# Kernel optimization log

Hardware: AMD Instinct MI355X
Metric: run time of the kernel (lower is better)

Reference implementation:

```python
import jax, jax.numpy as jnp
import numpy as np

B, L, D, H, DH, DFF, NL, A = 32, 1024, 512, 8, 64, 2048, 6, 21
CL = 4  # new variables per clique (chain junction tree)


def _build_mask():
    # Mirrors _make_junction_tree_mask: each position attends to itself,
    # to all parent-clique variables, and to earlier vars in its own clique.
    m = np.zeros((L, L), dtype=bool)
    for c in range(L // CL):
        own = range(c * CL, (c + 1) * CL)
        par = range((c - 1) * CL, c * CL) if c > 0 else range(0)
        for i in own:
            m[i, i] = True
            for p in par:
                m[i, p] = True
            for v in own:
                if v < i:
                    m[i, v] = True
    return m


def setup_inputs() -> dict:
    key = jax.random.key(0)
    ks = jax.random.split(key, 12)
    s = 0.02
    inp = {
        "x": jax.random.randint(ks[0], (B, L), 0, A, dtype=jnp.int32),
        "mask": jnp.asarray(_build_mask())[None, None],  # (1,1,L,L), broadcasts over B,H
        "tok_emb": jax.random.normal(ks[1], (A, D)) * s,
        "pos_emb": jax.random.normal(ks[2], (L, D)) * s,
        "wq": jax.random.normal(ks[3], (NL, D, D)) * s,
        "bq": jnp.zeros((NL, D)),
        "wk": jax.random.normal(ks[4], (NL, D, D)) * s,
        "bk": jnp.zeros((NL, D)),
        "wv": jax.random.normal(ks[5], (NL, D, D)) * s,
        "bv": jnp.zeros((NL, D)),
        "wo": jax.random.normal(ks[6], (NL, D, D)) * s,
        "bo": jnp.zeros((NL, D)),
        "ln1_s": jnp.ones((NL, D)),
        "ln1_b": jnp.zeros((NL, D)),
        "ln2_s": jnp.ones((NL, D)),
        "ln2_b": jnp.zeros((NL, D)),
        "w1": jax.random.normal(ks[7], (NL, D, DFF)) * s,
        "b1": jnp.zeros((NL, DFF)),
        "w2": jax.random.normal(ks[8], (NL, DFF, D)) * s,
        "b2": jnp.zeros((NL, D)),
        "wout": jax.random.normal(ks[9], (D, A)) * s,
        "bout": jnp.zeros((A,)),
    }
    return inp


def _ln(x, s, b):
    mu = x.mean(-1, keepdims=True)
    var = ((x - mu) ** 2).mean(-1, keepdims=True)
    return (x - mu) * jax.lax.rsqrt(var + 1e-6) * s + b


def reference(x, mask, tok_emb, pos_emb, wq, bq, wk, bk, wv, bv, wo, bo,
              ln1_s, ln1_b, ln2_s, ln2_b, w1, b1, w2, b2, wout, bout):
    h = tok_emb[x] + pos_emb[None, :, :]           # (B, L, D)
    neg = jnp.asarray(-1e9, h.dtype)
    scale = jnp.asarray(1.0 / np.sqrt(DH), h.dtype)
    for l in range(NL):
        # masked multi-head self-attention (pre-LN block)
        hn = _ln(h, ln1_s[l], ln1_b[l])
        q = (hn @ wq[l] + bq[l]).reshape(B, L, H, DH)
        k = (hn @ wk[l] + bk[l]).reshape(B, L, H, DH)
        v = (hn @ wv[l] + bv[l]).reshape(B, L, H, DH)
        sc = jnp.einsum('blhd,bmhd->bhlm', q, k) * scale
        sc = jnp.where(mask, sc, neg)              # junction-tree sparsity pattern
        attn = jax.nn.softmax(sc, axis=-1)
        o = jnp.einsum('bhlm,bmhd->blhd', attn, v).reshape(B, L, D) @ wo[l] + bo[l]
        h = h + o
        # feed-forward
        hn = _ln(h, ln2_s[l], ln2_b[l])
        h = h + (jax.nn.gelu(hn @ w1[l] + b1[l]) @ w2[l] + b2[l])
    return h @ wout + bout                          # (B, L, alphabet_size)
```

## Files before the change

### kernel.cpp

```cpp
#include <hip/hip_runtime.h>

#define BB 32
#define LL 1024
#define DD 512
#define HH 8
#define DHH 64
#define DFF 2048
#define NLAYERS 6
#define AA 21
#define MTOT (BB*LL)
#define QS 1536

typedef unsigned short u16;
typedef __bf16 bf16x8 __attribute__((ext_vector_type(8)));
typedef float f32x4 __attribute__((ext_vector_type(4)));
typedef u16 u16x8 __attribute__((ext_vector_type(8)));

__device__ __forceinline__ float bf2f(u16 u) {
    return __uint_as_float(((unsigned int)u) << 16);
}
__device__ __forceinline__ u16 f2bf(float f) {
    unsigned int i = __float_as_uint(f);
    unsigned int r = i + 0x7FFFu + ((i >> 16) & 1u);
    return (u16)(r >> 16);
}

__global__ void detect_kernel(const void* __restrict__ tok, int* __restrict__ flag) {
    __shared__ int cnt[256];
    int t = threadIdx.x;
    const u16* p = (const u16*)tok;
    int c = 0;
    #pragma unroll
    for (int j = 0; j < 8; j++) {
        u16 u = p[2 * (t * 8 + j)];
        int e = (u >> 7) & 0xFF;
        c += (e >= 97 && e <= 137) ? 1 : 0;
    }
    cnt[t] = c;
    __syncthreads();
    for (int s = 128; s; s >>= 1) {
        if (t < s) cnt[t] += cnt[t + s];
        __syncthreads();
    }
    if (t == 0) flag[0] = (cnt[0] > 1024) ? 1 : 0;
}

#define NTAB 13
struct ConvTab {
    const void* src[NTAB];
    unsigned long long dstOff[NTAB];
    int n[NTAB];
    int chunk[NTAB];
    int lstride[NTAB];
};
__global__ __launch_bounds__(256) void conv_small(ConvTab tab, u16* __restrict__ spBase,
                                                  const int* __restrict__ flag, int total) {
    int i = blockIdx.x * 256 + threadIdx.x;
    if (i >= total) return;
    int fl = flag[0];
    #pragma unroll 1
    for (int e = 0; e < NTAB; e++) {
        if (i < tab.n[e]) {
            const void* s = tab.src[e];
            u16 val = fl ? ((const u16*)s)[i] : f2bf(((const float*)s)[i]);
            int c = i / tab.chunk[e];
            int r = i - c * tab.chunk[e];
            spBase[tab.dstOff[e] + (size_t)c * tab.lstride[e] + r] = val;
            return;
        }
        i -= tab.n[e];
    }
}

__global__ __launch_bounds__(256) void conv_T(const void* __restrict__ src,
                                              u16* __restrict__ dst, int R, int C,
                                              const int* __restrict__ flag, int dstZS) {
    __shared__ u16 tile[32][33];
    int z = blockIdx.z;
    size_t zoffS = (size_t)z * R * C;
    size_t zoffD = (size_t)z * dstZS;
    int bx = blockIdx.x * 32, by = blockIdx.y * 32;
    int tx = threadIdx.x & 31, ty = threadIdx.x >> 5;
    int fl = flag[0];
    const u16* s16 = (const u16*)src + zoffS;
    const float* s32 = (const float*)src + zoffS;
    #pragma unroll
    for (int r = 0; r < 4; r++) {
        size_t idx = (size_t)(by + ty * 4 + r) * C + bx + tx;
        tile[ty * 4 + r][tx] = fl ? s16[idx] : f2bf(s32[idx]);
    }
    __syncthreads();
    #pragma unroll
    for (int r = 0; r < 4; r++)
        dst[zoffD + (size_t)(bx + ty * 4 + r) * R + by + tx] = tile[tx][ty * 4 + r];
}

__global__ __launch_bounds__(256) void woutpad_kernel(const void* __restrict__ wout,
                                                      const void* __restrict__ bout,
                                                      u16* __restrict__ wpad,
                                                      u16* __restrict__ bpad,
                                                      const int* __restrict__ flag) {
    int i = blockIdx.x * 256 + threadIdx.x;
    int fl = flag[0];
    if (i < 128 * 512) {
        int n = i >> 9, kk = i & 511;
        u16 val = 0;
        if (n < AA) val = fl ? ((const u16*)wout)[kk * AA + n] : f2bf(((const float*)wout)[kk * AA + n]);
        wpad[(size_t)n * 512 + kk] = val;
    }
    if (i < 128) {
        u16 val = 0;
        if (i < AA) val = fl ? ((const u16*)bout)[i] : f2bf(((const float*)bout)[i]);
        bpad[i] = val;
    }
}

__global__ __launch_bounds__(128) void embed_kernel(const int* __restrict__ x,
                                                    const u16* __restrict__ tok_emb,
                                                    const u16* __restrict__ pos_emb,
                                                    float* __restrict__ h) {
    int row = blockIdx.x;
    int l = row & (LL - 1);
    int tok = x[row];
    int c = threadIdx.x * 4;
    ushort4 te = *(const ushort4*)(tok_emb + (size_t)tok * DD + c);
    ushort4 pe = *(const ushort4*)(pos_emb + (size_t)l * DD + c);
    float4 o;
    o.x = bf2f(te.x) + bf2f(pe.x);
    o.y = bf2f(te.y) + bf2f(pe.y);
    o.z = bf2f(te.z) + bf2f(pe.z);
    o.w = bf2f(te.w) + bf2f(pe.w);
    *(float4*)(h + (size_t)row * DD + c) = o;
}

__global__ __launch_bounds__(256) void ln_kernel(const float* __restrict__ h,
                                                 const u16* __restrict__ s,
                                                 const u16* __restrict__ b,
                                                 u16* __restrict__ outp) {
    int row = blockIdx.x * 4 + (threadIdx.x >> 6);
    int lane = threadIdx.x & 63;
    const float* hr = h + (size_t)row * DD + lane * 8;
    f32x4 v0 = *(const f32x4*)hr;
    f32x4 v1 = *(const f32x4*)(hr + 4);
    float sum = v0[0]+v0[1]+v0[2]+v0[3]+v1[0]+v1[1]+v1[2]+v1[3];
    #pragma unroll
    for (int off = 32; off; off >>= 1) sum += __shfl_xor(sum, off, 64);
    float mu = sum * (1.0f / DD);
    float var = 0.f;
    #pragma unroll
    for (int i = 0; i < 4; i++) {
        float d0 = v0[i] - mu, d1 = v1[i] - mu;
        var += d0 * d0 + d1 * d1;
    }
    #pragma unroll
    for (int off = 32; off; off >>= 1) var += __shfl_xor(var, off, 64);
    float rs = rsqrtf(var * (1.0f / DD) + 1e-6f);
    u16x8 sv = *(const u16x8*)(s + lane * 8);
    u16x8 bv = *(const u16x8*)(b + lane * 8);
    u16x8 o;
    #pragma unroll
    for (int i = 0; i < 8; i++) {
        float xv = (i < 4) ? v0[i] : v1[i - 4];
        o[i] = f2bf((xv - mu) * rs * bf2f(sv[i]) + bf2f(bv[i]));
    }
    *(u16x8*)(outp + (size_t)row * DD + lane * 8) = o;
}

#define GLD16(gp, lp) __builtin_amdgcn_global_load_lds( \
    (const __attribute__((address_space(1))) void*)(gp), \
    (__attribute__((address_space(3))) void*)(lp), 16, 0, 0)

template <int EPI>
__global__ __launch_bounds__(256) void gemm_bt(const u16* __restrict__ A,
                                               const u16* __restrict__ BT,
                                               const u16* __restrict__ bias,
                                               u16* __restrict__ Cb,
                                               float* __restrict__ Cf,
                                               int M, int N, int K, int lda,
                                               const int* __restrict__ flag) {
    __shared__ __align__(16) u16 Als[2][128 * 32];
    __shared__ __align__(16) u16 Bls[2][128 * 32];
    const int tid  = threadIdx.x;
    const int lane = tid & 63;
    const int wave = tid >> 6;

    int gx = gridDim.x, gy = gridDim.y;
    int tileX, tileY;
    if ((gy & 7) == 0) {
        int bid = blockIdx.y * gx + blockIdx.x;
        int xcd = bid & 7;
        int idx = bid >> 3;
        int stripe = gy >> 3;
        tileX = idx % gx;
        tileY = xcd * stripe + idx / gx;
    } else {
        tileX = blockIdx.x; tileY = blockIdx.y;
    }
    const int tileM = tileY * 128;
    const int tileN = tileX * 128;
    const int wm = (wave & 1) * 64;
    const int wn = (wave >> 1) * 64;

    const int srow = tid >> 2;
    const int scol = (((tid & 3) ^ ((tid >> 3) & 3))) * 8;

    const u16* Ag0 = A  + (size_t)(tileM + srow) * lda + scol;
    const u16* Ag1 = A  + (size_t)(tileM + 64 + srow) * lda + scol;
    const u16* Bg0 = BT + (size_t)(tileN + srow) * K + scol;
    const u16* Bg1 = BT + (size_t)(tileN + 64 + srow) * K + scol;

    f32x4 acc[4][4] = {};
    const int lm = lane & 15;
    const int lk = (((lane >> 4) ^ ((lm >> 1) & 3))) * 8;

    const int nk = K >> 5;
    GLD16(Ag0, Als[0] + tid * 8);
    GLD16(Ag1, Als[0] + 2048 + tid * 8);
    GLD16(Bg0, Bls[0] + tid * 8);
    GLD16(Bg1, Bls[0] + 2048 + tid * 8);
    __syncthreads();

    for (int kt = 0; kt < nk; kt++) {
        const int cur = kt & 1;
        const int nxt = cur ^ 1;
        if (kt + 1 < nk) {
            const int k1 = (kt + 1) << 5;
            GLD16(Ag0 + k1, Als[nxt] + tid * 8);
            GLD16(Ag1 + k1, Als[nxt] + 2048 + tid * 8);
            GLD16(Bg0 + k1, Bls[nxt] + tid * 8);
            GLD16(Bg1 + k1, Bls[nxt] + 2048 + tid * 8);
        }
        bf16x8 af[4], bfr[4];
        #pragma unroll
        for (int i = 0; i < 4; i++)
            af[i] = *(const bf16x8*)(Als[cur] + (wm + i * 16 + lm) * 32 + lk);
        #pragma unroll
        for (int j = 0; j < 4; j++)
            bfr[j] = *(const bf16x8*)(Bls[cur] + (wn + j * 16 + lm) * 32 + lk);
        #pragma unroll
        for (int i = 0; i < 4; i++)
            #pragma unroll
            for (int j = 0; j < 4; j++)
                acc[i][j] = __builtin_amdgcn_mfma_f32_16x16x32_bf16(af[i], bfr[j], acc[i][j], 0, 0, 0);
        __syncthreads();
    }

    int fl = 0;
    if constexpr (EPI == 3) fl = flag[0];
    const int r0 = (lane >> 4) * 4;
    #pragma unroll
    for (int j = 0; j < 4; j++) {
        int col = tileN + wn + j * 16 + lm;
        float bv = bf2f(bias[col]);
        #pragma unroll
        for (int i = 0; i < 4; i++) {
            int row = tileM + wm + i * 16 + r0;
            #pragma unroll
            for (int r = 0; r < 4; r++) {
                float xv = acc[i][j][r] + bv;
                if constexpr (EPI == 0) {
                    Cb[(size_t)(row + r) * N + col] = f2bf(xv);
                } else if constexpr (EPI == 1) {
                    float u = 1.5957691216057308f * (xv + 0.044715f * xv * xv * xv);
                    float t = 1.0f - 2.0f / (__expf(u) + 1.0f);
                    Cb[(size_t)(row + r) * N + col] = f2bf(0.5f * xv * (1.0f + t));
                } else if constexpr (EPI == 2) {
                    Cf[(size_t)(row + r) * N + col] += xv;
                } else if constexpr (EPI == 4) {
                    size_t idx = (size_t)(row + r) * N + col;
                    Cb[idx] = f2bf(xv + Cf[idx]);
                } else {
                    if (col < AA) {
                        size_t idx = (size_t)(row + r) * AA + col;
                        if (fl) Cb[idx] = f2bf(xv);
                        else    Cf[idx] = xv;
                    }
                }
            }
        }
    }
}

__global__ __launch_bounds__(256) void attn_kernel(u16* qkv) {
    int bl   = blockIdx.x * 4 + (threadIdx.x >> 6);
    int lane = threadIdx.x & 63;
    int l    = bl & (LL - 1);
    int lo   = (l & ~3) - 4; if (lo < 0) lo = 0;
    int nj   = l - lo + 1;

    size_t qrow = (size_t)bl * QS;
    int off = lane * 8;

    u16x8 q8 = *(const u16x8*)(qkv + qrow + off);
    float qf[8];
    #pragma unroll
    for (int i = 0; i < 8; i++) qf[i] = bf2f(q8[i]) * 0.125f;

    size_t base = (size_t)(bl - (l - lo)) * QS;
    float sc[8];
    u16x8 v8[8];
    #pragma unroll
    for (int j = 0; j < 8; j++) {
        int jc = (j < nj) ? j : (nj - 1);
        const u16* krow = qkv + base + (size_t)jc * QS;
        u16x8 k8 = *(const u16x8*)(krow + 512 + off);
        v8[j]    = *(const u16x8*)(krow + 1024 + off);
        float t = 0.f;
        #pragma unroll
        for (int i = 0; i < 8; i++) t = fmaf(qf[i], bf2f(k8[i]), t);
        t += __shfl_xor(t, 1, 64);
        t += __shfl_xor(t, 2, 64);
        t += __shfl_xor(t, 4, 64);
        sc[j] = (j < nj) ? t : -1e30f;
    }
    float m = sc[0];
    #pragma unroll
    for (int j = 1; j < 8; j++) m = fmaxf(m, sc[j]);
    float p[8], den = 0.f;
    #pragma unroll
    for (int j = 0; j < 8; j++) { p[j] = __expf(sc[j] - m); den += p[j]; }
    float inv = 1.0f / den;
    float o[8] = {};
    #pragma unroll
    for (int j = 0; j < 8; j++)
        #pragma unroll
        for (int i = 0; i < 8; i++) o[i] = fmaf(p[j], bf2f(v8[j][i]), o[i]);
    u16x8 ov;
    #pragma unroll
    for (int i = 0; i < 8; i++) ov[i] = f2bf(o[i] * inv);
    *(u16x8*)(qkv + qrow + off) = ov;
}

extern "C" void kernel_launch(void* const* d_in, const int* in_sizes, int n_in,
                              void* d_out, int out_size, void* d_ws, size_t ws_size,
                              hipStream_t stream) {
    const int base = n_in - 22;
    const int*  x    = (const int*)d_in[0];
    const void* tokI = d_in[2 + base];
    const void* posI = d_in[3 + base];
    const void* wqI  = d_in[4 + base];
    const void* bqI  = d_in[5 + base];
    const void* wkI  = d_in[6 + base];
    const void* bkI  = d_in[7 + base];
    const void* wvI  = d_in[8 + base];
    const void* bvI  = d_in[9 + base];
    const void* woI  = d_in[10 + base];
    const void* boI  = d_in[11 + base];
    const void* ln1sI = d_in[12 + base];
    const void* ln1bI = d_in[13 + base];
    const void* ln2sI = d_in[14 + base];
    const void* ln2bI = d_in[15 + base];
    const void* w1I  = d_in[16 + base];
    const void* b1I  = d_in[17 + base];
    const void* w2I  = d_in[18 + base];
    const void* b2I  = d_in[19 + base];
    const void* woutI = d_in[20 + base];
    const void* boutI = d_in[21 + base];

    char* ws = (char*)d_ws;
    float* h   = (float*)(ws + 0);
    u16*  hn   = (u16*)(ws + 67108864);
    u16*  qkv  = (u16*)(ws + 100663296);
    u16*  wT   = (u16*)(ws + 201326592);
    u16*  sp   = (u16*)(ws + 239075328);
    int* flag  = (int*)(ws + 240500736);

    u16* mid = qkv;

    u16* wqkvT = wT;
    u16* woT   = wT + 4718592;
    u16* w1T   = wT + 6291456;
    u16* w2T   = wT + 12582912;

    const unsigned long long oWoutPad = 0;
    const unsigned long long oBoutPad = 65536;
    const unsigned long long oTok     = 65664;
    const unsigned long long oPos     = 76416;
    const unsigned long long oQkvB    = 600704;
    const unsigned long long oBo      = 609920;
    const unsigned long long oB1      = 612992;
    const unsigned long long oB2      = 625280;
    const unsigned long long oLn1s    = 628352;
    const unsigned long long oLn1b    = 631424;
    const unsigned long long oLn2s    = 634496;
    const unsigned long long oLn2b    = 637568;

    detect_kernel<<<1, 256, 0, stream>>>(tokI, flag);

    ConvTab tab;
    const void* srcs[NTAB] = {tokI, bqI, bkI, bvI, boI, b1I, b2I, ln1sI, ln1bI, ln2sI, ln2bI, posI, tokI};
    unsigned long long offs[NTAB] = {oTok, oQkvB, oQkvB + 512, oQkvB + 1024, oBo, oB1, oB2,
                                     oLn1s, oLn1b, oLn2s, oLn2b, oPos, oTok};
    int ns[NTAB]     = {10752, 3072, 3072, 3072, 3072, 12288, 3072, 3072, 3072, 3072, 3072, 524288, 0};
    int chunks[NTAB] = {10752, 512, 512, 512, 3072, 12288, 3072, 3072, 3072, 3072, 3072, 524288, 1};
    int lstr[NTAB]   = {10752, 1536, 1536, 1536, 3072, 12288, 3072, 3072, 3072, 3072, 3072, 524288, 1};
    int total = 0;
    for (int e = 0; e < NTAB; e++) {
        tab.src[e] = srcs[e]; tab.dstOff[e] = offs[e]; tab.n[e] = ns[e];
        tab.chunk[e] = chunks[e]; tab.lstride[e] = lstr[e];
        total += ns[e];
    }
    conv_small<<<(total + 255) / 256, 256, 0, stream>>>(tab, sp, flag, total);
    woutpad_kernel<<<256, 256, 0, stream>>>(woutI, boutI, sp + oWoutPad, sp + oBoutPad, flag);

    conv_T<<<dim3(16, 16, 6), 256, 0, stream>>>(wqI, wqkvT,          DD, DD, flag, 786432);
    conv_T<<<dim3(16, 16, 6), 256, 0, stream>>>(wkI, wqkvT + 262144, DD, DD, flag, 786432);
    conv_T<<<dim3(16, 16, 6), 256, 0, stream>>>(wvI, wqkvT + 524288, DD, DD, flag, 786432);
    conv_T<<<dim3(16, 16, 6), 256, 0, stream>>>(woI, woT, DD, DD, flag, 262144);
    conv_T<<<dim3(64, 16, 6), 256, 0, stream>>>(w1I, w1T, DD, DFF, flag, 1048576);
    conv_T<<<dim3(16, 64, 6), 256, 0, stream>>>(w2I, w2T, DFF, DD, flag, 1048576);

    embed_kernel<<<MTOT, 128, 0, stream>>>(x, sp + oTok, sp + oPos, h);

    for (int l = 0; l < NLAYERS; l++) {
        u16* wqkvTl = wqkvT + (size_t)l * 786432;
        u16* woTl   = woT + (size_t)l * 262144;
        u16* w1Tl   = w1T + (size_t)l * 1048576;
        u16* w2Tl   = w2T + (size_t)l * 1048576;

        ln_kernel<<<MTOT / 4, 256, 0, stream>>>(h, sp + oLn1s + l * DD, sp + oLn1b + l * DD, hn);

        gemm_bt<0><<<dim3(QS / 128, MTOT / 128), 256, 0, stream>>>(
            hn, wqkvTl, sp + oQkvB + l * QS, qkv, nullptr, MTOT, QS, DD, DD, flag);

        attn_kernel<<<MTOT / 4, 256, 0, stream>>>(qkv);

        gemm_bt<2><<<dim3(DD / 128, MTOT / 128), 256, 0, stream>>>(
            qkv, woTl, sp + oBo + l * DD, nullptr, h, MTOT, DD, DD, QS, flag);

        ln_kernel<<<MTOT / 4, 256, 0, stream>>>(h, sp + oLn2s + l * DD, sp + oLn2b + l * DD, hn);

        for (int half = 0; half < 2; half++) {
            const u16* Ahn = hn + (size_t)half * 16384 * DD;
            float* hHalf = h + (size_t)half * 16384 * DD;
            gemm_bt<1><<<dim3(DFF / 128, 16384 / 128), 256, 0, stream>>>(
                Ahn, w1Tl, sp + oB1 + l * DFF, mid, nullptr, 16384, DFF, DD, DD, flag);
            if (l < NLAYERS - 1) {
                gemm_bt<2><<<dim3(DD / 128, 16384 / 128), 256, 0, stream>>>(
                    mid, w2Tl, sp + oB2 + l * DD, nullptr, hHalf, 16384, DD, DFF, DFF, flag);
            } else {
                gemm_bt<4><<<dim3(DD / 128, 16384 / 128), 256, 0, stream>>>(
                    mid, w2Tl, sp + oB2 + l * DD, hn + (size_t)half * 16384 * DD, hHalf,
                    16384, DD, DFF, DFF, flag);
            }
        }
    }

    gemm_bt<3><<<dim3(1, MTOT / 128), 256, 0, stream>>>(
        hn, sp + oWoutPad, sp + oBoutPad, (u16*)d_out, (float*)d_out, MTOT, 128, DD, DD, flag);
}
```

Baseline: 2.752 ms.

## Add 256-wide tiled GEMM with 4-stage async LDS pipeline for transformer matmuls

Introduces a new GEMM kernel with 512 threads, 256x256 (or 128x256) tiles, a 4-buffer direct global-to-LDS load pipeline with explicit vmcnt waits, swizzled LDS layout, XCD-aware tile remapping and MFMA priority hints. It replaces the 128x128 gemm_bt for the QKV, output projection and both FFN matmuls. The aim is more data reuse per tile and better overlap of loads with MFMA work. The trade-off is fewer blocks per GEMM, which hurts wave quantization on the smaller N=512 GEMMs, plus higher register and LDS pressure.

```diff
diff --git a/kernel.cpp b/kernel.cpp
--- a/kernel.cpp
+++ b/kernel.cpp
@@ -281,6 +281,122 @@
     }
 }
 
+#define WAIT_VM(n) asm volatile("s_waitcnt vmcnt(" #n ") lgkmcnt(0)" ::: "memory")
+
+template <int EPI, int MREP>
+__global__ __launch_bounds__(512, 2) void gemm256(const u16* __restrict__ A,
+                                                  const u16* __restrict__ BT,
+                                                  const u16* __restrict__ bias,
+                                                  u16* __restrict__ Cb,
+                                                  float* __restrict__ Cf,
+                                                  int M, int N, int K, int lda,
+                                                  const int* __restrict__ flag) {
+    constexpr int BM = MREP * 32;
+    constexpr int ATILE = BM * 32;
+    constexpr int G = (MREP == 8) ? 4 : 3;
+    __shared__ __align__(16) u16 Als[4][ATILE];
+    __shared__ __align__(16) u16 Bls[4][256 * 32];
+
+    const int tid  = threadIdx.x;
+    const int lane = tid & 63;
+    const int wave = tid >> 6;
+    const int wm = wave & 1;
+    const int wn = wave >> 1;
+
+    int gx = gridDim.x, gy = gridDim.y;
+    int tileX, tileY;
+    if ((gy & 7) == 0) {
+        int bid = blockIdx.y * gx + blockIdx.x;
+        int xcd = bid & 7;
+        int idx = bid >> 3;
+        int stripe = gy >> 3;
+        tileX = idx % gx;
+        tileY = xcd * stripe + idx / gx;
+    } else {
+        tileX = blockIdx.x; tileY = blockIdx.y;
+    }
+    const int tileM = tileY * BM;
+    const int tileN = tileX * 256;
+
+    const int srow = tid >> 2;
+    const int scol = ((tid & 3) ^ ((tid >> 3) & 3)) * 8;
+    const u16* Ag0 = A  + (size_t)(tileM + srow) * lda + scol;
+    const u16* Bg0 = BT + (size_t)(tileN + srow) * K + scol;
+
+    auto STAGE = [&](int kt) {
+        const int buf = kt & 3;
+        const int ko = kt << 5;
+        GLD16(Ag0 + ko, Als[buf] + tid * 8);
+        if constexpr (MREP == 8)
+            GLD16(Ag0 + (size_t)128 * lda + ko, Als[buf] + 4096 + tid * 8);
+        GLD16(Bg0 + ko, Bls[buf] + tid * 8);
+        GLD16(Bg0 + (size_t)128 * K + ko, Bls[buf] + 4096 + tid * 8);
+    };
+
+    f32x4 acc[MREP][4] = {};
+    const int lm = lane & 15;
+    const int lk = ((lane >> 4) ^ ((lm >> 1) & 3)) * 8;
+    const int aoff = (wm * (MREP * 16) + lm) * 32 + lk;
+    const int boff = (wn * 64 + lm) * 32 + lk;
+    const int nk = K >> 5;
+
+    STAGE(0); STAGE(1); STAGE(2);
+    if constexpr (G == 4) WAIT_VM(8); else WAIT_VM(6);
+    __builtin_amdgcn_s_barrier();
+
+    for (int kt = 0; kt < nk; kt++) {
+        if (kt + 3 < nk) STAGE(kt + 3);
+        const u16* Ab = Als[kt & 3] + aoff;
+        const u16* Bb = Bls[kt & 3] + boff;
+        bf16x8 af[MREP], bfr[4];
+        #pragma unroll
+        for (int i = 0; i < MREP; i++) af[i] = *(const bf16x8*)(Ab + i * 16 * 32);
+        #pragma unroll
+        for (int j = 0; j < 4; j++)    bfr[j] = *(const bf16x8*)(Bb + j * 16 * 32);
+        __builtin_amdgcn_s_setprio(1);
+        #pragma unroll
+        for (int i = 0; i < MREP; i++)
+            #pragma unroll
+            for (int j = 0; j < 4; j++)
+                acc[i][j] = __builtin_amdgcn_mfma_f32_16x16x32_bf16(af[i], bfr[j], acc[i][j], 0, 0, 0);
+        __builtin_amdgcn_s_setprio(0);
+        if (kt + 1 < nk) {
+            if (kt + 3 < nk)      { if constexpr (G == 4) WAIT_VM(8); else WAIT_VM(6); }
+            else if (kt + 2 < nk) { if constexpr (G == 4) WAIT_VM(4); else WAIT_VM(3); }
+            else                  WAIT_VM(0);
+            __builtin_amdgcn_s_barrier();
+        }
+    }
+
+    (void)flag;
+    const int r0 = (lane >> 4) * 4;
+    #pragma unroll
+    for (int j = 0; j < 4; j++) {
+        int col = tileN + wn * 64 + j * 16 + lm;
+        float bvf = bf2f(bias[col]);
+        #pragma unroll
+        for (int i = 0; i < MREP; i++) {
+            int row = tileM + wm * (MREP * 16) + i * 16 + r0;
+            #pragma unroll
+            for (int r = 0; r < 4; r++) {
+                float xv = acc[i][j][r] + bvf;
+                if constexpr (EPI == 0) {
+                    Cb[(size_t)(row + r) * N + col] = f2bf(xv);
+                } else if constexpr (EPI == 1) {
+                    float u = 1.5957691216057308f * (xv + 0.044715f * xv * xv * xv);
+                    float t = 1.0f - 2.0f / (__expf(u) + 1.0f);
+                    Cb[(size_t)(row + r) * N + col] = f2bf(0.5f * xv * (1.0f + t));
+                } else if constexpr (EPI == 2) {
+                    Cf[(size_t)(row + r) * N + col] += xv;
+                } else if constexpr (EPI == 4) {
+                    size_t idx = (size_t)(row + r) * N + col;
+                    Cb[idx] = f2bf(xv + Cf[idx]);
+                }
+            }
+        }
+    }
+}
+
 __global__ __launch_bounds__(256) void attn_kernel(u16* qkv) {
     int bl   = blockIdx.x * 4 + (threadIdx.x >> 6);
     int lane = threadIdx.x & 63;
@@ -420,12 +536,12 @@
 
         ln_kernel<<<MTOT / 4, 256, 0, stream>>>(h, sp + oLn1s + l * DD, sp + oLn1b + l * DD, hn);
 
-        gemm_bt<0><<<dim3(QS / 128, MTOT / 128), 256, 0, stream>>>(
+        gemm256<0, 8><<<dim3(QS / 256, MTOT / 256), 512, 0, stream>>>(
             hn, wqkvTl, sp + oQkvB + l * QS, qkv, nullptr, MTOT, QS, DD, DD, flag);
 
         attn_kernel<<<MTOT / 4, 256, 0, stream>>>(qkv);
 
-        gemm_bt<2><<<dim3(DD / 128, MTOT / 128), 256, 0, stream>>>(
+        gemm256<2, 8><<<dim3(DD / 256, MTOT / 256), 512, 0, stream>>>(
             qkv, woTl, sp + oBo + l * DD, nullptr, h, MTOT, DD, DD, QS, flag);
 
         ln_kernel<<<MTOT / 4, 256, 0, stream>>>(h, sp + oLn2s + l * DD, sp + oLn2b + l * DD, hn);
@@ -433,13 +549,13 @@
         for (int half = 0; half < 2; half++) {
             const u16* Ahn = hn + (size_t)half * 16384 * DD;
             float* hHalf = h + (size_t)half * 16384 * DD;
-            gemm_bt<1><<<dim3(DFF / 128, 16384 / 128), 256, 0, stream>>>(
+            gemm256<1, 8><<<dim3(DFF / 256, 16384 / 256), 512, 0, stream>>>(
                 Ahn, w1Tl, sp + oB1 + l * DFF, mid, nullptr, 16384, DFF, DD, DD, flag);
             if (l < NLAYERS - 1) {
-                gemm_bt<2><<<dim3(DD / 128, 16384 / 128), 256, 0, stream>>>(
+                gemm256<2, 4><<<dim3(DD / 256, 16384 / 128), 512, 0, stream>>>(
                     mid, w2Tl, sp + oB2 + l * DD, nullptr, hHalf, 16384, DD, DFF, DFF, flag);
             } else {
-                gemm_bt<4><<<dim3(DD / 128, 16384 / 128), 256, 0, stream>>>(
+                gemm256<4, 4><<<dim3(DD / 256, 16384 / 128), 512, 0, stream>>>(
                     mid, w2Tl, sp + oB2 + l * DD, hn + (size_t)half * 16384 * DD, hHalf,
                     16384, DD, DFF, DFF, flag);
             }
```

Result: slower. 3.023 ms (+9.9%).

## Use three-stage LDS pipeline with partial vmcnt waits in GEMM

Applied to the files above, without the earlier changes.

The GEMM main loop goes from double-buffered to triple-buffered LDS staging. Tiles are prefetched two k-steps ahead, and the full syncthreads is replaced by an explicit s_waitcnt vmcnt(4) plus s_barrier, so one stage of global-to-LDS loads can stay in flight across the barrier. This aims to hide global load latency better. It costs 50% more shared memory per block, which may reduce occupancy, and correctness now relies on the hand-written waitcnt counts.

```diff
diff --git a/kernel.cpp b/kernel.cpp
--- a/kernel.cpp
+++ b/kernel.cpp
@@ -169,6 +169,7 @@
 #define GLD16(gp, lp) __builtin_amdgcn_global_load_lds( \
     (const __attribute__((address_space(1))) void*)(gp), \
     (__attribute__((address_space(3))) void*)(lp), 16, 0, 0)
+#define WAIT_VM(n) asm volatile("s_waitcnt vmcnt(" #n ") lgkmcnt(0)" ::: "memory")
 
 template <int EPI>
 __global__ __launch_bounds__(256) void gemm_bt(const u16* __restrict__ A,
@@ -178,8 +179,8 @@
                                                float* __restrict__ Cf,
                                                int M, int N, int K, int lda,
                                                const int* __restrict__ flag) {
-    __shared__ __align__(16) u16 Als[2][128 * 32];
-    __shared__ __align__(16) u16 Bls[2][128 * 32];
+    __shared__ __align__(16) u16 Als[3][128 * 32];
+    __shared__ __align__(16) u16 Bls[3][128 * 32];
     const int tid  = threadIdx.x;
     const int lane = tid & 63;
     const int wave = tid >> 6;
@@ -214,21 +215,29 @@
     const int lk = (((lane >> 4) ^ ((lm >> 1) & 3))) * 8;
 
     const int nk = K >> 5;
-    GLD16(Ag0, Als[0] + tid * 8);
-    GLD16(Ag1, Als[0] + 2048 + tid * 8);
-    GLD16(Bg0, Bls[0] + tid * 8);
-    GLD16(Bg1, Bls[0] + 2048 + tid * 8);
-    __syncthreads();
-
+
+    {
+        GLD16(Ag0, Als[0] + tid * 8);
+        GLD16(Ag1, Als[0] + 2048 + tid * 8);
+        GLD16(Bg0, Bls[0] + tid * 8);
+        GLD16(Bg1, Bls[0] + 2048 + tid * 8);
+        GLD16(Ag0 + 32, Als[1] + tid * 8);
+        GLD16(Ag1 + 32, Als[1] + 2048 + tid * 8);
+        GLD16(Bg0 + 32, Bls[1] + tid * 8);
+        GLD16(Bg1 + 32, Bls[1] + 2048 + tid * 8);
+    }
+    WAIT_VM(4);
+    __builtin_amdgcn_s_barrier();
+
+    int cur = 0;
+    int stg = 2;
     for (int kt = 0; kt < nk; kt++) {
-        const int cur = kt & 1;
-        const int nxt = cur ^ 1;
-        if (kt + 1 < nk) {
-            const int k1 = (kt + 1) << 5;
-            GLD16(Ag0 + k1, Als[nxt] + tid * 8);
-            GLD16(Ag1 + k1, Als[nxt] + 2048 + tid * 8);
-            GLD16(Bg0 + k1, Bls[nxt] + tid * 8);
-            GLD16(Bg1 + k1, Bls[nxt] + 2048 + tid * 8);
+        if (kt + 2 < nk) {
+            const int k2 = (kt + 2) << 5;
+            GLD16(Ag0 + k2, Als[stg] + tid * 8);
+            GLD16(Ag1 + k2, Als[stg] + 2048 + tid * 8);
+            GLD16(Bg0 + k2, Bls[stg] + tid * 8);
+            GLD16(Bg1 + k2, Bls[stg] + 2048 + tid * 8);
         }
         bf16x8 af[4], bfr[4];
         #pragma unroll
@@ -242,7 +251,13 @@
             #pragma unroll
             for (int j = 0; j < 4; j++)
                 acc[i][j] = __builtin_amdgcn_mfma_f32_16x16x32_bf16(af[i], bfr[j], acc[i][j], 0, 0, 0);
-        __syncthreads();
+        if (kt + 1 < nk) {
+            if (kt + 2 < nk) WAIT_VM(4);
+            else             WAIT_VM(0);
+            __builtin_amdgcn_s_barrier();
+        }
+        cur = (cur == 2) ? 0 : cur + 1;
+        stg = (stg == 2) ? 0 : stg + 1;
     }
 
     int fl = 0;
```

New measurement: 2.833 ms. +3.0%, slower.
